# Kernel tuning notes

Measured on AMD Instinct MI355X. Metric: run time of the kernel, lower is better.

Reference implementation:

```python
import jax, jax.numpy as jnp
import numpy as np

B, D, C_IN, C_OUT = 256, 8, 2, 4


def setup_inputs() -> dict:
    key = jax.random.key(0)
    k1, k2, k3, k4 = jax.random.split(key, 4)
    rho = jax.random.normal(k1, (B, C_IN * D * D, C_IN * D * D), dtype=jnp.float32)
    ux = jax.random.normal(k2, (D, D), dtype=jnp.float32)
    uy = jax.random.normal(k3, (D, D), dtype=jnp.float32)
    uc = jax.random.normal(k4, (C_OUT, C_OUT), dtype=jnp.float32)
    return {"rho": rho, "ux": ux, "uy": uy, "uc": uc}


def _insert_channels(rho, d, c_in, c_out):
    # Faithful port of _InsertChannels: move each (channel f, pixel i,j) row/col
    # index to channel f + (c_out - c_in) in the enlarged register.
    b = rho.shape[0]
    x = jnp.arange(c_in * d * d)
    f = x // (d * d)                       # channel index
    i = (x % (d * d)) // d                 # row pixel
    j = x % d                              # col pixel
    new_idx = i * d + j + (f + (c_out - c_in)) * d * d  # [c_in*d^2]
    big = jnp.zeros((b, c_out * d * d, c_out * d * d), dtype=rho.dtype)
    # Indices are a bijection onto a sub-block, so add == set (matches
    # index_put_(..., accumulate=True) in torch).
    return big.at[:, new_idx[:, None], new_idx[None, :]].add(rho)


def reference(rho, ux, uy, uc):
    d = ux.shape[0]
    c_out = uc.shape[0]
    c_in = rho.shape[1] // (d * d)
    # channel insertion (c_in < c_out path)
    rho_big = _insert_channels(rho, d, c_in, c_out)        # [b, C, C], C = c_out*d^2
    # u = kron(uc, kron(ux, uy))
    u = jnp.kron(uc, jnp.kron(ux, uy))                     # [C, C]
    # new_rho = u @ rho @ u^H (real float32 -> conj is identity, transpose only)
    u_rho = jnp.einsum('pq,bqr->bpr', u, rho_big)
    new_rho = jnp.einsum('bpr,sr->bps', u_rho, u)
    return new_rho
```

## Files before the change

kernel.cpp:

```cpp
#include <hip/hip_runtime.h>


#define TPB 512

typedef float nfloat4 __attribute__((ext_vector_type(4)));

__global__ __launch_bounds__(TPB, 2) void qconv_fused(
    const float* __restrict__ rho,
    const float* __restrict__ ux,
    const float* __restrict__ uy,
    const float* __restrict__ uc,
    float* __restrict__ out)
{
    __shared__ alignas(16) float L[4][64][68];

    const int tid  = threadIdx.x;
    const int b    = blockIdx.x;
    const int w    = tid >> 6;
    const int lane = tid & 63;
    const int pyp  = lane >> 3, qyp = lane & 7;

    const int qg  = tid & 15;
    const int csh = (tid >> 4) & 1;
    const int spl = tid >> 5;

    float e0[4], e1[4];
#pragma unroll
    for (int c = 0; c < 4; ++c) { e0[c] = uc[c*4+2]; e1[c] = uc[c*4+3]; }
    float* ob = out + (size_t)b * 65536;

    float X[64];

    if (w < 4) {
        const int c1 = w >> 1, c2 = w & 1;
        const int px = lane >> 3, qx = lane & 7;
        const float* rb = rho + (size_t)b * 16384
                        + (size_t)((c1 << 6) + (px << 3)) * 128 + (c2 << 6) + (qx << 3);

#pragma unroll
        for (int py = 0; py < 8; ++py) {
            float4 lo = *(const float4*)(rb + py * 128);
            float4 hi = *(const float4*)(rb + py * 128 + 4);
            X[py*8+0]=lo.x; X[py*8+1]=lo.y; X[py*8+2]=lo.z; X[py*8+3]=lo.w;
            X[py*8+4]=hi.x; X[py*8+5]=hi.y; X[py*8+6]=hi.z; X[py*8+7]=hi.w;
        }

#pragma unroll
        for (int r = 0; r < 8; ++r) {
            float t[8];
#pragma unroll
            for (int j = 0; j < 8; ++j) {
                float a = 0.f;
#pragma unroll
                for (int k = 0; k < 8; ++k) a += uy[j*8+k] * X[r*8+k];
                t[j] = a;
            }
#pragma unroll
            for (int j = 0; j < 8; ++j) X[r*8+j] = t[j];
        }

#pragma unroll
        for (int cc = 0; cc < 8; ++cc) {
            float t[8];
#pragma unroll
            for (int i = 0; i < 8; ++i) {
                float a = 0.f;
#pragma unroll
                for (int k = 0; k < 8; ++k) a += uy[i*8+k] * X[k*8+cc];
                t[i] = a;
            }
#pragma unroll
            for (int i = 0; i < 8; ++i) X[i*8+cc] = t[i];
        }

#pragma unroll
        for (int e = 0; e < 64; ++e)
            L[w][e][lane ^ (((e >> 3) & 7) << 2)] = X[e];
        __asm__ volatile("s_waitcnt lgkmcnt(0)" ::: "memory");
        {
            const int sw = ((lane >> 3) & 7) << 2;
#pragma unroll
            for (int f4 = 0; f4 < 16; ++f4) {
                float4 v = *(const float4*)&L[w][lane][(f4 * 4) ^ sw];
                X[f4*4+0]=v.x; X[f4*4+1]=v.y; X[f4*4+2]=v.z; X[f4*4+3]=v.w;
            }
        }

#pragma unroll
        for (int p = 0; p < 8; ++p) {
            float t[8];
#pragma unroll
            for (int j = 0; j < 8; ++j) {
                float a = 0.f;
#pragma unroll
                for (int k = 0; k < 8; ++k) a += ux[j*8+k] * X[p*8+k];
                t[j] = a;
            }
#pragma unroll
            for (int j = 0; j < 8; ++j) X[p*8+j] = t[j];
        }
    }

#pragma unroll
    for (int s = 0; s < 4; ++s) {
        if (w < 4) {
#pragma unroll
            for (int i2 = 0; i2 < 2; ++i2) {
                const int i = 2*s + i2;
#pragma unroll
                for (int j = 0; j < 8; ++j) {
                    float acc = 0.f;
#pragma unroll
                    for (int k = 0; k < 8; ++k) acc += ux[i*8+k] * X[k*8+j];
                    L[w][i*8+pyp][j*8+qyp] = acc;
                }
            }
        }
        __asm__ volatile("s_waitcnt lgkmcnt(0)" ::: "memory");
        __builtin_amdgcn_s_barrier();
        __asm__ volatile("" ::: "memory");

        const int sp = 16*s + spl;
        float4 wv[4];
#pragma unroll
        for (int ww = 0; ww < 4; ++ww) wv[ww] = *(const float4*)&L[ww][sp][qg * 4];
#pragma unroll
        for (int c = 0; c < 4; ++c) {
#pragma unroll
            for (int cs2 = 0; cs2 < 2; ++cs2) {
                const int cs = 2*csh + cs2;
                const float k00 = e0[c]*e0[cs], k01 = e0[c]*e1[cs];
                const float k10 = e1[c]*e0[cs], k11 = e1[c]*e1[cs];
                nfloat4 v;
                v.x = k00*wv[0].x + k01*wv[1].x + k10*wv[2].x + k11*wv[3].x;
                v.y = k00*wv[0].y + k01*wv[1].y + k10*wv[2].y + k11*wv[3].y;
                v.z = k00*wv[0].z + k01*wv[1].z + k10*wv[2].z + k11*wv[3].z;
                v.w = k00*wv[0].w + k01*wv[1].w + k10*wv[2].w + k11*wv[3].w;
                __builtin_nontemporal_store(v,
                    (nfloat4*)&ob[(size_t)((c*64 + sp) * 256 + cs*64 + qg*4)]);
            }
        }
    }
}

extern "C" void kernel_launch(void* const* d_in, const int* in_sizes, int n_in,
                              void* d_out, int out_size, void* d_ws, size_t ws_size,
                              hipStream_t stream) {
    const float* rho = (const float*)d_in[0];
    const float* ux  = (const float*)d_in[1];
    const float* uy  = (const float*)d_in[2];
    const float* uc  = (const float*)d_in[3];
    float* out = (float*)d_out;
    qconv_fused<<<dim3(256), dim3(TPB), 0, stream>>>(rho, ux, uy, uc, out);
}
```

Measured before the change: 89.97 us.

## Split fused kernel into two launches, staging intermediate through output buffer

Splits the single fused kernel (256 blocks of 512 threads) into two kernels. The first runs 1024 single-wave blocks that each apply the uy/ux transforms to one channel quadrant and write the result into the output's first 64 rows. The second runs 2048 blocks that read those rows back and expand them across channels with the uc coefficients. The aim is more parallelism and better occupancy than the original, where only 4 of 8 waves did the transform work. In exchange it adds a second launch and a global-memory round trip for the intermediate, and the stage-2 blocks overwrite the rows they read, which depends on each block's reads finishing before its own writes.

```diff
diff --git a/kernel.cpp b/kernel.cpp
--- a/kernel.cpp
+++ b/kernel.cpp
@@ -1,144 +1,141 @@
 #include <hip/hip_runtime.h>
 
 
-#define TPB 512
-
 typedef float nfloat4 __attribute__((ext_vector_type(4)));
 
-__global__ __launch_bounds__(TPB, 2) void qconv_fused(
+__global__ __launch_bounds__(64) void qconv_stage1(
     const float* __restrict__ rho,
     const float* __restrict__ ux,
     const float* __restrict__ uy,
-    const float* __restrict__ uc,
     float* __restrict__ out)
 {
-    __shared__ alignas(16) float L[4][64][68];
+    __shared__ alignas(16) float T[64][68];
 
-    const int tid  = threadIdx.x;
-    const int b    = blockIdx.x;
-    const int w    = tid >> 6;
-    const int lane = tid & 63;
-    const int pyp  = lane >> 3, qyp = lane & 7;
+    const int lane = threadIdx.x;
+    const int b    = blockIdx.x & 255;
+    const int quad = blockIdx.x >> 8;
+    const int c1 = quad >> 1, c2 = quad & 1;
+    const int px = lane >> 3, qx = lane & 7;
 
-    const int qg  = tid & 15;
+    const float* rb = rho + (size_t)b * 16384
+                    + (size_t)((c1 << 6) + (px << 3)) * 128 + (c2 << 6) + (qx << 3);
+
+    float X[64];
+#pragma unroll
+    for (int py = 0; py < 8; ++py) {
+        float4 lo = *(const float4*)(rb + py * 128);
+        float4 hi = *(const float4*)(rb + py * 128 + 4);
+        X[py*8+0]=lo.x; X[py*8+1]=lo.y; X[py*8+2]=lo.z; X[py*8+3]=lo.w;
+        X[py*8+4]=hi.x; X[py*8+5]=hi.y; X[py*8+6]=hi.z; X[py*8+7]=hi.w;
+    }
+
+#pragma unroll
+    for (int r = 0; r < 8; ++r) {
+        float t[8];
+#pragma unroll
+        for (int j = 0; j < 8; ++j) {
+            float a = 0.f;
+#pragma unroll
+            for (int k = 0; k < 8; ++k) a += uy[j*8+k] * X[r*8+k];
+            t[j] = a;
+        }
+#pragma unroll
+        for (int j = 0; j < 8; ++j) X[r*8+j] = t[j];
+    }
+
+#pragma unroll
+    for (int cc = 0; cc < 8; ++cc) {
+        float t[8];
+#pragma unroll
+        for (int i = 0; i < 8; ++i) {
+            float a = 0.f;
+#pragma unroll
+            for (int k = 0; k < 8; ++k) a += uy[i*8+k] * X[k*8+cc];
+            t[i] = a;
+        }
+#pragma unroll
+        for (int i = 0; i < 8; ++i) X[i*8+cc] = t[i];
+    }
+
+#pragma unroll
+    for (int e = 0; e < 64; ++e)
+        T[e][lane ^ (((e >> 3) & 7) << 2)] = X[e];
+    __asm__ volatile("s_waitcnt lgkmcnt(0)" ::: "memory");
+    {
+        const int sw = ((lane >> 3) & 7) << 2;
+#pragma unroll
+        for (int f4 = 0; f4 < 16; ++f4) {
+            float4 v = *(const float4*)&T[lane][(f4 * 4) ^ sw];
+            X[f4*4+0]=v.x; X[f4*4+1]=v.y; X[f4*4+2]=v.z; X[f4*4+3]=v.w;
+        }
+    }
+
+#pragma unroll
+    for (int p = 0; p < 8; ++p) {
+        float t[8];
+#pragma unroll
+        for (int j = 0; j < 8; ++j) {
+            float a = 0.f;
+#pragma unroll
+            for (int k = 0; k < 8; ++k) a += ux[j*8+k] * X[p*8+k];
+            t[j] = a;
+        }
+#pragma unroll
+        for (int j = 0; j < 8; ++j) X[p*8+j] = t[j];
+    }
+
+    float* ob = out + (size_t)b * 65536;
+    const int pyp = lane >> 3, qyp = lane & 7;
+#pragma unroll
+    for (int i = 0; i < 8; ++i) {
+#pragma unroll
+        for (int j = 0; j < 8; ++j) {
+            float acc = 0.f;
+#pragma unroll
+            for (int k = 0; k < 8; ++k) acc += ux[i*8+k] * X[k*8+j];
+            ob[(size_t)(i*8 + pyp) * 256 + quad * 64 + j*8 + qyp] = acc;
+        }
+    }
+}
+
+__global__ __launch_bounds__(256, 8) void qconv_stage2(
+    const float* __restrict__ uc,
+    float* out)
+{
+    const int tid = threadIdx.x;
+    const int b   = blockIdx.x & 255;
+    const int z   = blockIdx.x >> 8;
+    const int q   = tid & 15;
     const int csh = (tid >> 4) & 1;
-    const int spl = tid >> 5;
+    const int p   = z * 8 + (tid >> 5);
 
     float e0[4], e1[4];
 #pragma unroll
     for (int c = 0; c < 4; ++c) { e0[c] = uc[c*4+2]; e1[c] = uc[c*4+3]; }
+
     float* ob = out + (size_t)b * 65536;
 
-    float X[64];
+    nfloat4 wv[4];
+#pragma unroll
+    for (int quad = 0; quad < 4; ++quad)
+        wv[quad] = *(const nfloat4*)(ob + (size_t)p * 256 + quad * 64 + q * 4);
 
-    if (w < 4) {
-        const int c1 = w >> 1, c2 = w & 1;
-        const int px = lane >> 3, qx = lane & 7;
-        const float* rb = rho + (size_t)b * 16384
-                        + (size_t)((c1 << 6) + (px << 3)) * 128 + (c2 << 6) + (qx << 3);
+    __syncthreads();
 
+    float* obp = ob + (size_t)p * 256 + q * 4;
 #pragma unroll
-        for (int py = 0; py < 8; ++py) {
-            float4 lo = *(const float4*)(rb + py * 128);
-            float4 hi = *(const float4*)(rb + py * 128 + 4);
-            X[py*8+0]=lo.x; X[py*8+1]=lo.y; X[py*8+2]=lo.z; X[py*8+3]=lo.w;
-            X[py*8+4]=hi.x; X[py*8+5]=hi.y; X[py*8+6]=hi.z; X[py*8+7]=hi.w;
-        }
-
+    for (int c = 0; c < 4; ++c) {
 #pragma unroll
-        for (int r = 0; r < 8; ++r) {
-            float t[8];
-#pragma unroll
-            for (int j = 0; j < 8; ++j) {
-                float a = 0.f;
-#pragma unroll
-                for (int k = 0; k < 8; ++k) a += uy[j*8+k] * X[r*8+k];
-                t[j] = a;
-            }
-#pragma unroll
-            for (int j = 0; j < 8; ++j) X[r*8+j] = t[j];
-        }
-
-#pragma unroll
-        for (int cc = 0; cc < 8; ++cc) {
-            float t[8];
-#pragma unroll
-            for (int i = 0; i < 8; ++i) {
-                float a = 0.f;
-#pragma unroll
-                for (int k = 0; k < 8; ++k) a += uy[i*8+k] * X[k*8+cc];
-                t[i] = a;
-            }
-#pragma unroll
-            for (int i = 0; i < 8; ++i) X[i*8+cc] = t[i];
-        }
-
-#pragma unroll
-        for (int e = 0; e < 64; ++e)
-            L[w][e][lane ^ (((e >> 3) & 7) << 2)] = X[e];
-        __asm__ volatile("s_waitcnt lgkmcnt(0)" ::: "memory");
-        {
-            const int sw = ((lane >> 3) & 7) << 2;
-#pragma unroll
-            for (int f4 = 0; f4 < 16; ++f4) {
-                float4 v = *(const float4*)&L[w][lane][(f4 * 4) ^ sw];
-                X[f4*4+0]=v.x; X[f4*4+1]=v.y; X[f4*4+2]=v.z; X[f4*4+3]=v.w;
-            }
-        }
-
-#pragma unroll
-        for (int p = 0; p < 8; ++p) {
-            float t[8];
-#pragma unroll
-            for (int j = 0; j < 8; ++j) {
-                float a = 0.f;
-#pragma unroll
-                for (int k = 0; k < 8; ++k) a += ux[j*8+k] * X[p*8+k];
-                t[j] = a;
-            }
-#pragma unroll
-            for (int j = 0; j < 8; ++j) X[p*8+j] = t[j];
-        }
-    }
-
-#pragma unroll
-    for (int s = 0; s < 4; ++s) {
-        if (w < 4) {
-#pragma unroll
-            for (int i2 = 0; i2 < 2; ++i2) {
-                const int i = 2*s + i2;
-#pragma unroll
-                for (int j = 0; j < 8; ++j) {
-                    float acc = 0.f;
-#pragma unroll
-                    for (int k = 0; k < 8; ++k) acc += ux[i*8+k] * X[k*8+j];
-                    L[w][i*8+pyp][j*8+qyp] = acc;
-                }
-            }
-        }
-        __asm__ volatile("s_waitcnt lgkmcnt(0)" ::: "memory");
-        __builtin_amdgcn_s_barrier();
-        __asm__ volatile("" ::: "memory");
-
-        const int sp = 16*s + spl;
-        float4 wv[4];
-#pragma unroll
-        for (int ww = 0; ww < 4; ++ww) wv[ww] = *(const float4*)&L[ww][sp][qg * 4];
-#pragma unroll
-        for (int c = 0; c < 4; ++c) {
-#pragma unroll
-            for (int cs2 = 0; cs2 < 2; ++cs2) {
-                const int cs = 2*csh + cs2;
-                const float k00 = e0[c]*e0[cs], k01 = e0[c]*e1[cs];
-                const float k10 = e1[c]*e0[cs], k11 = e1[c]*e1[cs];
-                nfloat4 v;
-                v.x = k00*wv[0].x + k01*wv[1].x + k10*wv[2].x + k11*wv[3].x;
-                v.y = k00*wv[0].y + k01*wv[1].y + k10*wv[2].y + k11*wv[3].y;
-                v.z = k00*wv[0].z + k01*wv[1].z + k10*wv[2].z + k11*wv[3].z;
-                v.w = k00*wv[0].w + k01*wv[1].w + k10*wv[2].w + k11*wv[3].w;
-                __builtin_nontemporal_store(v,
-                    (nfloat4*)&ob[(size_t)((c*64 + sp) * 256 + cs*64 + qg*4)]);
-            }
+        for (int cs2 = 0; cs2 < 2; ++cs2) {
+            const int cs = 2 * csh + cs2;
+            const float k00 = e0[c]*e0[cs], k01 = e0[c]*e1[cs];
+            const float k10 = e1[c]*e0[cs], k11 = e1[c]*e1[cs];
+            nfloat4 v;
+            v.x = k00*wv[0].x + k01*wv[1].x + k10*wv[2].x + k11*wv[3].x;
+            v.y = k00*wv[0].y + k01*wv[1].y + k10*wv[2].y + k11*wv[3].y;
+            v.z = k00*wv[0].z + k01*wv[1].z + k10*wv[2].z + k11*wv[3].z;
+            v.w = k00*wv[0].w + k01*wv[1].w + k10*wv[2].w + k11*wv[3].w;
+            __builtin_nontemporal_store(v, (nfloat4*)(obp + c * 16384 + cs * 64));
         }
     }
 }
@@ -151,5 +148,7 @@
     const float* uy  = (const float*)d_in[2];
     const float* uc  = (const float*)d_in[3];
     float* out = (float*)d_out;
-    qconv_fused<<<dim3(256), dim3(TPB), 0, stream>>>(rho, ux, uy, uc, out);
+
+    qconv_stage1<<<dim3(1024), dim3(64),  0, stream>>>(rho, ux, uy, out);
+    qconv_stage2<<<dim3(2048), dim3(256), 0, stream>>>(uc, out);
 }
```

Result: slower. 98.78 us (+9.8%).
